# Kernel optimization log

Measured on AMD Instinct MI355X. Metric: run time of the kernel, lower is better.

## Reference

```python
import jax, jax.numpy as jnp
import numpy as np

# ---- configuration matching GeoBleuSinkhornLoss init_kwargs ----
H, W = 200, 200            # grid -> V = H*W = 40000
WIN = 7                    # neighbor window, K = 49
BETA = 0.5
CELL_X, CELL_Y = 0.5, 0.5
DSCALE = 2.0
EPS = 0.1
N_ITERS = 30
N_LIST = (1, 2, 3, 4, 5)
B, T = 16, 96
V = H * W


def setup_inputs() -> dict:
    key = jax.random.key(0)
    k1, k2 = jax.random.split(key)
    logits = jax.random.normal(k1, (B, T, V), dtype=jnp.float32)
    target_ids = jax.random.randint(k2, (B, T), 0, V)
    # physical-distance kernel (make_local_offsets_physical)
    r = WIN // 2
    dy, dx = np.meshgrid(np.arange(-r, r + 1), np.arange(-r, r + 1), indexing='ij')
    offsets = jnp.asarray(np.stack([dy, dx], axis=-1).reshape(-1, 2), dtype=jnp.int32)  # (K,2)
    dist_km = np.hypot(dy * CELL_Y, dx * CELL_X) * DSCALE
    kernel_w = jnp.asarray(np.exp(-BETA * dist_km).reshape(-1), dtype=jnp.float32)      # (K,)
    ngram_weights = jnp.full((len(N_LIST),), 1.0 / len(N_LIST), dtype=jnp.float32)
    return dict(logits=logits, kernel_w=kernel_w, ngram_weights=ngram_weights,
                target_ids=target_ids, offsets=offsets)


def _sinkhorn(S):
    # entropic-OT row/col scaling: M = diag(a) K diag(b)
    Bm, I, J = S.shape
    Kmat = jnp.clip(jnp.exp(S / EPS), 1e-30, None)
    mu = jnp.full((Bm, I), 1.0 / I, dtype=S.dtype)
    nu = jnp.full((Bm, J), 1.0 / J, dtype=S.dtype)

    def step(carry, _):
        a, b = carry
        a = mu / jnp.clip(jnp.einsum('bij,bj->bi', Kmat, b), 1e-30, None)
        b = nu / jnp.clip(jnp.einsum('bij,bi->bj', Kmat, a), 1e-30, None)
        return (a, b), None

    (a, b), _ = jax.lax.scan(step, (jnp.ones_like(mu), jnp.ones_like(nu)),
                             None, length=N_ITERS)
    return a[:, :, None] * Kmat * b[:, None, :]


def reference(logits, kernel_w, ngram_weights, target_ids, offsets):
    p = jax.nn.softmax(logits, axis=-1)                     # (B,T,V)
    # neighbor ids + validity mask (id_to_rc / rc_to_id + clamp)
    r_u = target_ids // W                                   # (B,T)
    c_u = target_ids % W
    rn = r_u[..., None] + offsets[:, 0].astype(target_ids.dtype)   # (B,T,K)
    cn = c_u[..., None] + offsets[:, 1].astype(target_ids.dtype)
    valid = ((rn >= 0) & (rn < H) & (cn >= 0) & (cn < W)).astype(p.dtype)
    nb_ids = jnp.clip(rn, 0, H - 1) * W + jnp.clip(cn, 0, W - 1)   # (B,T,K)
    wts = valid * kernel_w                                   # (B,T,K)
    # U[b,t,u] = sum_k wts[b,u,k] * p[b,t, nb_ids[b,u,k]]   (vectorized gather)
    gathered = jnp.take_along_axis(p[:, :, None, :], nb_ids[:, None, :, :], axis=-1)  # (B,T,T,K)
    U = jnp.clip(jnp.einsum('btuk,buk->btu', gathered, wts), 1e-12, None)             # (B,T,T)

    loss_terms = []
    for wn, n in zip(ngram_weights, N_LIST):
        I = T - n + 1
        if I <= 0:
            continue
        # S[b,i,j] = prod_{k<n} U[b,i+k,j+k] via shifted-diagonal products
        S = U[:, :I, :I]
        for k in range(1, n):
            S = S * U[:, k:k + I, k:k + I]
        S = jnp.clip(S, 1e-12, None)
        M = _sinkhorn(S)
        q_n = jnp.clip(jnp.sum(M * S, axis=(-1, -2)) / I, 1e-12, None)  # (B,)
        loss_terms.append(-wn * jnp.log(q_n))
    loss = jnp.sum(jnp.stack(loss_terms, axis=0), axis=0).mean()
    return loss
```

## Files before the change

### kernel.cpp

```cpp
#include <hip/hip_runtime.h>
#include <math.h>

#define H_ 200
#define W_ 200
#define B_ 16
#define T_ 96
#define V_ 40000
#define K_ 49
#define NMAX_ 5
#define EPS_INV 10.0f
#define N_ITERS_ 30

__global__ __launch_bounds__(256) void fused_stream_U(const float* __restrict__ logits,
                                                      const int* __restrict__ target_ids,
                                                      const int* __restrict__ offsets,
                                                      const float* __restrict__ kernel_w,
                                                      float* __restrict__ Uo) {
    const int row = blockIdx.x;
    const int b = row / T_;
    const float* lrow = logits + (size_t)row * V_;

    __shared__ int s_off[2 * K_];
    __shared__ float s_kw[K_];
    __shared__ float ls[4];
    __shared__ float sh_inv;
    if (threadIdx.x < 2 * K_) s_off[threadIdx.x] = offsets[threadIdx.x];
    if (threadIdx.x >= 128 && threadIdx.x < 128 + K_) s_kw[threadIdx.x - 128] = kernel_w[threadIdx.x - 128];

    const float4* rp = (const float4*)lrow;
    float s0 = 0.f, s1 = 0.f, s2 = 0.f, s3 = 0.f;
    int i = threadIdx.x;
    for (int j = 0; j < 9; ++j) {
        float4 v0 = rp[i];
        float4 v1 = rp[i + 256];
        float4 v2 = rp[i + 512];
        float4 v3 = rp[i + 768];
        s0 += __expf(v0.x); s1 += __expf(v0.y); s2 += __expf(v0.z); s3 += __expf(v0.w);
        s0 += __expf(v1.x); s1 += __expf(v1.y); s2 += __expf(v1.z); s3 += __expf(v1.w);
        s0 += __expf(v2.x); s1 += __expf(v2.y); s2 += __expf(v2.z); s3 += __expf(v2.w);
        s0 += __expf(v3.x); s1 += __expf(v3.y); s2 += __expf(v3.z); s3 += __expf(v3.w);
        i += 1024;
    }
    {
        float4 v0 = rp[i];
        float4 v1 = rp[i + 256];
        float4 v2 = rp[i + 512];
        s0 += __expf(v0.x); s1 += __expf(v0.y); s2 += __expf(v0.z); s3 += __expf(v0.w);
        s0 += __expf(v1.x); s1 += __expf(v1.y); s2 += __expf(v1.z); s3 += __expf(v1.w);
        s0 += __expf(v2.x); s1 += __expf(v2.y); s2 += __expf(v2.z); s3 += __expf(v2.w);
    }
    if (threadIdx.x < 16) {
        float4 v3 = rp[9984 + threadIdx.x];
        s0 += __expf(v3.x); s1 += __expf(v3.y); s2 += __expf(v3.z); s3 += __expf(v3.w);
    }
    float s = (s0 + s1) + (s2 + s3);
    for (int off = 32; off > 0; off >>= 1) s += __shfl_down(s, off);
    if ((threadIdx.x & 63) == 0) ls[threadIdx.x >> 6] = s;
    __syncthreads();
    if (threadIdx.x == 0) sh_inv = 1.0f / ((ls[0] + ls[1]) + (ls[2] + ls[3]));
    __syncthreads();

    const int u = threadIdx.x;
    if (u < T_) {
        const int tgt = target_ids[b * T_ + u];
        const int ru = tgt / W_;
        const int cu = tgt - ru * W_;
        const float inv = sh_inv;
        float acc = 0.f;
        #pragma unroll
        for (int k = 0; k < K_; k++) {
            int rn = ru + s_off[2 * k];
            int cn = cu + s_off[2 * k + 1];
            bool val = (rn >= 0) & (rn < H_) & (cn >= 0) & (cn < W_);
            int rc = min(max(rn, 0), H_ - 1);
            int cc = min(max(cn, 0), W_ - 1);
            float w = val ? s_kw[k] : 0.f;
            acc += w * __expf(lrow[rc * W_ + cc]);
        }
        Uo[(size_t)row * T_ + u] = fmaxf(acc * inv, 1e-12f);
    }
}

__global__ __launch_bounds__(384) void sinkhorn_kernel(const float* __restrict__ U,
                                                       const float* __restrict__ ngw,
                                                       float* __restrict__ terms) {
    const int bi = blockIdx.x;
    const int b = bi / NMAX_;
    const int ni = bi - b * NMAX_;
    const int n = ni + 1;
    const int I = T_ - n + 1;

    __shared__ __align__(16) float Us[T_][T_ + 1];
    __shared__ __align__(16) float av[T_];
    __shared__ __align__(16) float bv[T_];
    __shared__ float rs[T_];

    const float* Ub = U + (size_t)b * T_ * T_;

    for (int idx = threadIdx.x; idx < T_ * T_; idx += 384) {
        int i = idx / T_;
        int j = idx - i * T_;
        Us[i][j] = Ub[idx];
    }
    if (threadIdx.x < T_) bv[threadIdx.x] = 1.0f;
    __syncthreads();

    const int r  = threadIdx.x >> 2;
    const int q4 = threadIdx.x & 3;
    const int c0 = q4 * 24;

    float kreg[24], ktreg[24], sreg[24];
    #pragma unroll
    for (int c = 0; c < 24; c++) {
        const int j = c0 + c;
        const bool ok = (r < I) & (j < I);
        float p1 = Us[r][j];
        float p2 = Us[j][r];
        #pragma unroll
        for (int k = 1; k < NMAX_; k++) {
            int rk = min(r + k, T_ - 1), jk = min(j + k, T_ - 1);
            if (k < n) {
                p1 *= Us[rk][jk];
                p2 *= Us[jk][rk];
            }
        }
        p1 = fmaxf(p1, 1e-12f);
        p2 = fmaxf(p2, 1e-12f);
        sreg[c]  = ok ? p1 : 0.f;
        kreg[c]  = ok ? fmaxf(__expf(p1 * EPS_INV), 1e-30f) : 0.f;
        ktreg[c] = ok ? fmaxf(__expf(p2 * EPS_INV), 1e-30f) : 0.f;
    }
    __syncthreads();

    const float muv = 1.0f / (float)I;
    const float2* bp = (const float2*)(bv + c0);
    const float2* ap = (const float2*)(av + c0);

    for (int it = 0; it < N_ITERS_; it++) {
        {
            float a0 = 0.f, a1 = 0.f, a2 = 0.f, a3 = 0.f;
            #pragma unroll
            for (int cc = 0; cc < 12; cc += 2) {
                float2 b0 = bp[cc], b1 = bp[cc + 1];
                a0 = fmaf(kreg[2 * cc],     b0.x, a0);
                a1 = fmaf(kreg[2 * cc + 1], b0.y, a1);
                a2 = fmaf(kreg[2 * cc + 2], b1.x, a2);
                a3 = fmaf(kreg[2 * cc + 3], b1.y, a3);
            }
            float acc = (a0 + a1) + (a2 + a3);
            acc += __shfl_xor(acc, 1);
            acc += __shfl_xor(acc, 2);
            if (q4 == 0) av[r] = muv / fmaxf(acc, 1e-30f);
        }
        __syncthreads();
        {
            float a0 = 0.f, a1 = 0.f, a2 = 0.f, a3 = 0.f;
            #pragma unroll
            for (int cc = 0; cc < 12; cc += 2) {
                float2 aa0 = ap[cc], aa1 = ap[cc + 1];
                a0 = fmaf(ktreg[2 * cc],     aa0.x, a0);
                a1 = fmaf(ktreg[2 * cc + 1], aa0.y, a1);
                a2 = fmaf(ktreg[2 * cc + 2], aa1.x, a2);
                a3 = fmaf(ktreg[2 * cc + 3], aa1.y, a3);
            }
            float acc = (a0 + a1) + (a2 + a3);
            acc += __shfl_xor(acc, 1);
            acc += __shfl_xor(acc, 2);
            if (q4 == 0) bv[r] = muv / fmaxf(acc, 1e-30f);
        }
        __syncthreads();
    }

    {
        float a0 = 0.f, a1 = 0.f;
        #pragma unroll
        for (int cc = 0; cc < 12; cc++) {
            float2 bb = bp[cc];
            a0 = fmaf(kreg[2 * cc]     * sreg[2 * cc],     bb.x, a0);
            a1 = fmaf(kreg[2 * cc + 1] * sreg[2 * cc + 1], bb.y, a1);
        }
        float acc = (a0 + a1) * av[r];
        acc += __shfl_xor(acc, 1);
        acc += __shfl_xor(acc, 2);
        if (q4 == 0) rs[r] = acc;
    }
    __syncthreads();
    if (threadIdx.x < 64) {
        float v = rs[threadIdx.x];
        if (threadIdx.x < 32) v += rs[64 + threadIdx.x];
        for (int off = 32; off > 0; off >>= 1) v += __shfl_down(v, off);
        if (threadIdx.x == 0) {
            float q = fmaxf(v / (float)I, 1e-12f);
            terms[bi] = -ngw[ni] * logf(q);
        }
    }
}

__global__ __launch_bounds__(128) void final_reduce(const float* __restrict__ terms,
                                                    float* __restrict__ out) {
    float acc = 0.f;
    if (threadIdx.x < B_ * NMAX_) acc = terms[threadIdx.x];
    for (int off = 32; off > 0; off >>= 1) acc += __shfl_down(acc, off);
    __shared__ float r2[2];
    if ((threadIdx.x & 63) == 0) r2[threadIdx.x >> 6] = acc;
    __syncthreads();
    if (threadIdx.x == 0) out[0] = (r2[0] + r2[1]) / (float)B_;
}

extern "C" void kernel_launch(void* const* d_in, const int* in_sizes, int n_in,
                              void* d_out, int out_size, void* d_ws, size_t ws_size,
                              hipStream_t stream) {
    const float* logits     = (const float*)d_in[0];
    const float* kernel_w   = (const float*)d_in[1];
    const float* ngram_w    = (const float*)d_in[2];
    const int*   target_ids = (const int*)d_in[3];
    const int*   offsets    = (const int*)d_in[4];
    float* out = (float*)d_out;

    float* ws   = (float*)d_ws;
    float* U    = ws;
    float* term = U + B_ * T_ * T_;

    fused_stream_U<<<B_ * T_, 256, 0, stream>>>(logits, target_ids, offsets, kernel_w, U);
    sinkhorn_kernel<<<B_ * NMAX_, 384, 0, stream>>>(U, ngram_w, term);
    final_reduce<<<1, 128, 0, stream>>>(term, out);
}
```

Baseline: 87.56 us.

## Software-pipeline softmax row loads and restructure Sinkhorn to 192 threads with shared K

The softmax-sum loop in the U kernel now prefetches the next batch of float4 loads before computing the exponentials of the current batch, and issues the tail loads early, to overlap memory latency with compute. The Sinkhorn kernel drops from 384 to 192 threads, with each thread covering 48 columns. It computes S and K once into shared-memory tiles and builds the transposed K from shared memory instead of recomputing the transposed products and exponentials. It also loads U with float4, uses a hardware reciprocal, and removes one shuffle stage. The trade-offs are fewer threads per Sinkhorn block, more registers per thread, and more shared memory.

```diff
diff --git a/kernel.cpp b/kernel.cpp
--- a/kernel.cpp
+++ b/kernel.cpp
@@ -10,6 +10,7 @@
 #define NMAX_ 5
 #define EPS_INV 10.0f
 #define N_ITERS_ 30
+#define LST 98
 
 __global__ __launch_bounds__(256) void fused_stream_U(const float* __restrict__ logits,
                                                       const int* __restrict__ target_ids,
@@ -18,51 +19,54 @@
                                                       float* __restrict__ Uo) {
     const int row = blockIdx.x;
     const int b = row / T_;
+    const int tid = threadIdx.x;
     const float* lrow = logits + (size_t)row * V_;
+    const float4* rp = (const float4*)lrow;
 
     __shared__ int s_off[2 * K_];
     __shared__ float s_kw[K_];
     __shared__ float ls[4];
     __shared__ float sh_inv;
-    if (threadIdx.x < 2 * K_) s_off[threadIdx.x] = offsets[threadIdx.x];
-    if (threadIdx.x >= 128 && threadIdx.x < 128 + K_) s_kw[threadIdx.x - 128] = kernel_w[threadIdx.x - 128];
-
-    const float4* rp = (const float4*)lrow;
+    if (tid < 2 * K_) s_off[tid] = offsets[tid];
+    if (tid >= 128 && tid < 128 + K_) s_kw[tid - 128] = kernel_w[tid - 128];
+
+    float4 r0 = rp[tid + 9216];
+    float4 r1 = rp[tid + 9472];
+    float4 r2 = rp[tid + 9728];
+    float4 a0 = rp[tid], a1 = rp[tid + 256], a2 = rp[tid + 512], a3 = rp[tid + 768];
+
     float s0 = 0.f, s1 = 0.f, s2 = 0.f, s3 = 0.f;
-    int i = threadIdx.x;
-    for (int j = 0; j < 9; ++j) {
-        float4 v0 = rp[i];
-        float4 v1 = rp[i + 256];
-        float4 v2 = rp[i + 512];
-        float4 v3 = rp[i + 768];
-        s0 += __expf(v0.x); s1 += __expf(v0.y); s2 += __expf(v0.z); s3 += __expf(v0.w);
-        s0 += __expf(v1.x); s1 += __expf(v1.y); s2 += __expf(v1.z); s3 += __expf(v1.w);
-        s0 += __expf(v2.x); s1 += __expf(v2.y); s2 += __expf(v2.z); s3 += __expf(v2.w);
-        s0 += __expf(v3.x); s1 += __expf(v3.y); s2 += __expf(v3.z); s3 += __expf(v3.w);
+    int i = tid + 1024;
+    #pragma unroll 2
+    for (int j = 0; j < 8; ++j) {
+        float4 b0 = rp[i], b1 = rp[i + 256], b2 = rp[i + 512], b3 = rp[i + 768];
         i += 1024;
-    }
-    {
-        float4 v0 = rp[i];
-        float4 v1 = rp[i + 256];
-        float4 v2 = rp[i + 512];
-        s0 += __expf(v0.x); s1 += __expf(v0.y); s2 += __expf(v0.z); s3 += __expf(v0.w);
-        s0 += __expf(v1.x); s1 += __expf(v1.y); s2 += __expf(v1.z); s3 += __expf(v1.w);
-        s0 += __expf(v2.x); s1 += __expf(v2.y); s2 += __expf(v2.z); s3 += __expf(v2.w);
-    }
-    if (threadIdx.x < 16) {
-        float4 v3 = rp[9984 + threadIdx.x];
-        s0 += __expf(v3.x); s1 += __expf(v3.y); s2 += __expf(v3.z); s3 += __expf(v3.w);
+        s0 += __expf(a0.x); s1 += __expf(a0.y); s2 += __expf(a0.z); s3 += __expf(a0.w);
+        s0 += __expf(a1.x); s1 += __expf(a1.y); s2 += __expf(a1.z); s3 += __expf(a1.w);
+        s0 += __expf(a2.x); s1 += __expf(a2.y); s2 += __expf(a2.z); s3 += __expf(a2.w);
+        s0 += __expf(a3.x); s1 += __expf(a3.y); s2 += __expf(a3.z); s3 += __expf(a3.w);
+        a0 = b0; a1 = b1; a2 = b2; a3 = b3;
+    }
+    s0 += __expf(a0.x); s1 += __expf(a0.y); s2 += __expf(a0.z); s3 += __expf(a0.w);
+    s0 += __expf(a1.x); s1 += __expf(a1.y); s2 += __expf(a1.z); s3 += __expf(a1.w);
+    s0 += __expf(a2.x); s1 += __expf(a2.y); s2 += __expf(a2.z); s3 += __expf(a2.w);
+    s0 += __expf(a3.x); s1 += __expf(a3.y); s2 += __expf(a3.z); s3 += __expf(a3.w);
+    s0 += __expf(r0.x); s1 += __expf(r0.y); s2 += __expf(r0.z); s3 += __expf(r0.w);
+    s0 += __expf(r1.x); s1 += __expf(r1.y); s2 += __expf(r1.z); s3 += __expf(r1.w);
+    s0 += __expf(r2.x); s1 += __expf(r2.y); s2 += __expf(r2.z); s3 += __expf(r2.w);
+    if (tid < 16) {
+        float4 t = rp[9984 + tid];
+        s0 += __expf(t.x); s1 += __expf(t.y); s2 += __expf(t.z); s3 += __expf(t.w);
     }
     float s = (s0 + s1) + (s2 + s3);
     for (int off = 32; off > 0; off >>= 1) s += __shfl_down(s, off);
-    if ((threadIdx.x & 63) == 0) ls[threadIdx.x >> 6] = s;
-    __syncthreads();
-    if (threadIdx.x == 0) sh_inv = 1.0f / ((ls[0] + ls[1]) + (ls[2] + ls[3]));
-    __syncthreads();
-
-    const int u = threadIdx.x;
-    if (u < T_) {
-        const int tgt = target_ids[b * T_ + u];
+    if ((tid & 63) == 0) ls[tid >> 6] = s;
+    __syncthreads();
+    if (tid == 0) sh_inv = 1.0f / ((ls[0] + ls[1]) + (ls[2] + ls[3]));
+    __syncthreads();
+
+    if (tid < T_) {
+        const int tgt = target_ids[b * T_ + tid];
         const int ru = tgt / W_;
         const int cu = tgt - ru * W_;
         const float inv = sh_inv;
@@ -77,11 +81,11 @@
             float w = val ? s_kw[k] : 0.f;
             acc += w * __expf(lrow[rc * W_ + cc]);
         }
-        Uo[(size_t)row * T_ + u] = fmaxf(acc * inv, 1e-12f);
-    }
-}
-
-__global__ __launch_bounds__(384) void sinkhorn_kernel(const float* __restrict__ U,
+        Uo[(size_t)row * T_ + tid] = fmaxf(acc * inv, 1e-12f);
+    }
+}
+
+__global__ __launch_bounds__(192) void sinkhorn_kernel(const float* __restrict__ U,
                                                        const float* __restrict__ ngw,
                                                        float* __restrict__ terms) {
     const int bi = blockIdx.x;
@@ -90,47 +94,50 @@
     const int n = ni + 1;
     const int I = T_ - n + 1;
 
-    __shared__ __align__(16) float Us[T_][T_ + 1];
-    __shared__ __align__(16) float av[T_];
-    __shared__ __align__(16) float bv[T_];
+    __shared__ __align__(16) float Us[T_][LST];
+    __shared__ __align__(16) float Ks[T_][LST];
+    __shared__ __align__(16) float Ss[T_][LST];
+    __shared__ __align__(16) float av[T_], bv[T_];
     __shared__ float rs[T_];
 
-    const float* Ub = U + (size_t)b * T_ * T_;
-
-    for (int idx = threadIdx.x; idx < T_ * T_; idx += 384) {
-        int i = idx / T_;
-        int j = idx - i * T_;
-        Us[i][j] = Ub[idx];
+    const float4* Ug = (const float4*)(U + (size_t)b * T_ * T_);
+    #pragma unroll
+    for (int m = 0; m < 12; m++) {
+        int idx = threadIdx.x + 192 * m;
+        float4 v = Ug[idx];
+        int fi = idx * 4;
+        int i = fi / T_;
+        int j = fi - i * T_;
+        *(float2*)&Us[i][j]     = make_float2(v.x, v.y);
+        *(float2*)&Us[i][j + 2] = make_float2(v.z, v.w);
     }
     if (threadIdx.x < T_) bv[threadIdx.x] = 1.0f;
     __syncthreads();
 
-    const int r  = threadIdx.x >> 2;
-    const int q4 = threadIdx.x & 3;
-    const int c0 = q4 * 24;
-
-    float kreg[24], ktreg[24], sreg[24];
-    #pragma unroll
-    for (int c = 0; c < 24; c++) {
+    const int r  = threadIdx.x >> 1;
+    const int p  = threadIdx.x & 1;
+    const int c0 = p * 48;
+
+    float kreg[48], ktreg[48];
+    #pragma unroll 8
+    for (int c = 0; c < 48; c++) {
         const int j = c0 + c;
         const bool ok = (r < I) & (j < I);
         float p1 = Us[r][j];
-        float p2 = Us[j][r];
         #pragma unroll
         for (int k = 1; k < NMAX_; k++) {
             int rk = min(r + k, T_ - 1), jk = min(j + k, T_ - 1);
-            if (k < n) {
-                p1 *= Us[rk][jk];
-                p2 *= Us[jk][rk];
-            }
+            if (k < n) p1 *= Us[rk][jk];
         }
         p1 = fmaxf(p1, 1e-12f);
-        p2 = fmaxf(p2, 1e-12f);
-        sreg[c]  = ok ? p1 : 0.f;
-        kreg[c]  = ok ? fmaxf(__expf(p1 * EPS_INV), 1e-30f) : 0.f;
-        ktreg[c] = ok ? fmaxf(__expf(p2 * EPS_INV), 1e-30f) : 0.f;
-    }
-    __syncthreads();
+        float kv = ok ? __expf(p1 * EPS_INV) : 0.f;
+        Ss[r][j] = ok ? p1 : 0.f;
+        Ks[r][j] = kv;
+        kreg[c] = kv;
+    }
+    __syncthreads();
+    #pragma unroll 8
+    for (int c = 0; c < 48; c++) ktreg[c] = Ks[c0 + c][r];
 
     const float muv = 1.0f / (float)I;
     const float2* bp = (const float2*)(bv + c0);
@@ -138,51 +145,50 @@
 
     for (int it = 0; it < N_ITERS_; it++) {
         {
-            float a0 = 0.f, a1 = 0.f, a2 = 0.f, a3 = 0.f;
+            float x0 = 0.f, x1 = 0.f, x2 = 0.f, x3 = 0.f;
             #pragma unroll
-            for (int cc = 0; cc < 12; cc += 2) {
+            for (int cc = 0; cc < 24; cc += 2) {
                 float2 b0 = bp[cc], b1 = bp[cc + 1];
-                a0 = fmaf(kreg[2 * cc],     b0.x, a0);
-                a1 = fmaf(kreg[2 * cc + 1], b0.y, a1);
-                a2 = fmaf(kreg[2 * cc + 2], b1.x, a2);
-                a3 = fmaf(kreg[2 * cc + 3], b1.y, a3);
+                x0 = fmaf(kreg[2 * cc],     b0.x, x0);
+                x1 = fmaf(kreg[2 * cc + 1], b0.y, x1);
+                x2 = fmaf(kreg[2 * cc + 2], b1.x, x2);
+                x3 = fmaf(kreg[2 * cc + 3], b1.y, x3);
             }
-            float acc = (a0 + a1) + (a2 + a3);
+            float acc = (x0 + x1) + (x2 + x3);
             acc += __shfl_xor(acc, 1);
-            acc += __shfl_xor(acc, 2);
-            if (q4 == 0) av[r] = muv / fmaxf(acc, 1e-30f);
+            if (p == 0) av[r] = muv * __builtin_amdgcn_rcpf(fmaxf(acc, 1e-30f));
         }
         __syncthreads();
         {
-            float a0 = 0.f, a1 = 0.f, a2 = 0.f, a3 = 0.f;
+            float x0 = 0.f, x1 = 0.f, x2 = 0.f, x3 = 0.f;
             #pragma unroll
-            for (int cc = 0; cc < 12; cc += 2) {
-                float2 aa0 = ap[cc], aa1 = ap[cc + 1];
-                a0 = fmaf(ktreg[2 * cc],     aa0.x, a0);
-                a1 = fmaf(ktreg[2 * cc + 1], aa0.y, a1);
-                a2 = fmaf(ktreg[2 * cc + 2], aa1.x, a2);
-                a3 = fmaf(ktreg[2 * cc + 3], aa1.y, a3);
+            for (int cc = 0; cc < 24; cc += 2) {
+                float2 a0 = ap[cc], a1 = ap[cc + 1];
+                x0 = fmaf(ktreg[2 * cc],     a0.x, x0);
+                x1 = fmaf(ktreg[2 * cc + 1], a0.y, x1);
+                x2 = fmaf(ktreg[2 * cc + 2], a1.x, x2);
+                x3 = fmaf(ktreg[2 * cc + 3], a1.y, x3);
             }
-            float acc = (a0 + a1) + (a2 + a3);
+            float acc = (x0 + x1) + (x2 + x3);
             acc += __shfl_xor(acc, 1);
-            acc += __shfl_xor(acc, 2);
-            if (q4 == 0) bv[r] = muv / fmaxf(acc, 1e-30f);
+            if (p == 0) bv[r] = muv * __builtin_amdgcn_rcpf(fmaxf(acc, 1e-30f));
         }
         __syncthreads();
     }
 
     {
-        float a0 = 0.f, a1 = 0.f;
+        const float2* sp = (const float2*)(&Ss[r][c0]);
+        float x0 = 0.f, x1 = 0.f;
         #pragma unroll
-        for (int cc = 0; cc < 12; cc++) {
+        for (int cc = 0; cc < 24; cc++) {
             float2 bb = bp[cc];
-            a0 = fmaf(kreg[2 * cc]     * sreg[2 * cc],     bb.x, a0);
-            a1 = fmaf(kreg[2 * cc + 1] * sreg[2 * cc + 1], bb.y, a1);
-        }
-        float acc = (a0 + a1) * av[r];
+            float2 sv = sp[cc];
+            x0 = fmaf(kreg[2 * cc]     * sv.x, bb.x, x0);
+            x1 = fmaf(kreg[2 * cc + 1] * sv.y, bb.y, x1);
+        }
+        float acc = (x0 + x1) * av[r];
         acc += __shfl_xor(acc, 1);
-        acc += __shfl_xor(acc, 2);
-        if (q4 == 0) rs[r] = acc;
+        if (p == 0) rs[r] = acc;
     }
     __syncthreads();
     if (threadIdx.x < 64) {
@@ -222,6 +228,6 @@
     float* term = U + B_ * T_ * T_;
 
     fused_stream_U<<<B_ * T_, 256, 0, stream>>>(logits, target_ids, offsets, kernel_w, U);
-    sinkhorn_kernel<<<B_ * NMAX_, 384, 0, stream>>>(U, ngram_w, term);
+    sinkhorn_kernel<<<B_ * NMAX_, 192, 0, stream>>>(U, ngram_w, term);
     final_reduce<<<1, 128, 0, stream>>>(term, out);
 }
```

Result: slower. 128.6 us (+46.9%).
